# Kernel optimization log

Hardware: AMD Instinct MI355X
Metric: run time of the kernel (lower is better)

Reference implementation:

```python
import jax, jax.numpy as jnp
import numpy as np

N_NODES = 100000
N_EDGES = 1600000
FEAT = 512
CLS = 64
HID = 200  # each hop layer output width; 3 hops -> 600 concat


def spmm(row, col, vals, x):
    # out[r] = sum_{e: row[e]==r} vals[e] * x[col[e]]  -- sparse A @ x
    return jax.ops.segment_sum(x[col] * vals[:, None], row, num_segments=x.shape[0])


def setup_inputs() -> dict:
    key = jax.random.key(0)
    ks = jax.random.split(key, 12)
    adj_index = jax.random.randint(ks[0], (2, N_EDGES), 0, N_NODES, dtype=jnp.int64)
    # scale like a normalized adjacency (~1/avg_degree) to keep powers stable
    adj_values = jax.random.uniform(ks[1], (N_EDGES,), dtype=jnp.float32) * (1.0 / 16.0)
    features = jax.random.normal(ks[2], (N_NODES, FEAT), dtype=jnp.float32)
    s1 = (2.0 / (FEAT + HID)) ** 0.5
    s2 = (2.0 / (3 * HID + HID)) ** 0.5
    sf = (2.0 / (3 * HID + CLS)) ** 0.5
    W1 = jax.random.normal(ks[3], (3, FEAT, HID), dtype=jnp.float32) * s1
    b1 = jax.random.normal(ks[4], (3, HID), dtype=jnp.float32) * 0.01
    W2 = jax.random.normal(ks[5], (3, 3 * HID, HID), dtype=jnp.float32) * s2
    b2 = jax.random.normal(ks[6], (3, HID), dtype=jnp.float32) * 0.01
    Wfc = jax.random.normal(ks[7], (3 * HID, CLS), dtype=jnp.float32) * sf
    bfc = jax.random.normal(ks[8], (CLS,), dtype=jnp.float32) * 0.01
    return {"adj_index": adj_index, "adj_values": adj_values, "features": features,
            "W1": W1, "b1": b1, "W2": W2, "b2": b2, "Wfc": Wfc, "bfc": bfc}


def reference(adj_index, adj_values, features, W1, b1, W2, b2, Wfc, bfc):
    # Inference mode: dropout is identity.
    row, col = adj_index[0], adj_index[1]
    # upper (sparse) layers: linear + bias + relu, then (iterations-1) spmm hops
    outs1 = []
    for i in range(3):  # iterations = i + 1
        h = jax.nn.relu(features @ W1[i] + b1[i][None, :])
        for _ in range(i):
            h = spmm(row, col, adj_values, h)
        outs1.append(h)
    abstract1 = jnp.concatenate(outs1, axis=1)  # [N, 600]
    # bottom (dense) layers: linear, (iterations-1) spmm hops, then + bias
    outs2 = []
    for i in range(3):
        h = abstract1 @ W2[i]
        for _ in range(i):
            h = spmm(row, col, adj_values, h)
        h = h + b2[i][None, :]
        outs2.append(h)
    abstract2 = jnp.concatenate(outs2, axis=1)  # [N, 600]
    node_emb = abstract2 @ Wfc + bfc  # [N, CLS]
    predictions = jax.nn.log_softmax(node_emb, axis=1)
    return node_emb, predictions
```

## Files before the change

kernel.cpp:

```cpp
#include <hip/hip_runtime.h>

typedef unsigned short u16;
typedef unsigned int u32;
typedef __attribute__((ext_vector_type(8))) short short8;
typedef __attribute__((ext_vector_type(4))) float f32x4;
typedef __attribute__((ext_vector_type(4))) u32 u32x4;
typedef __attribute__((ext_vector_type(2))) u32 u32x2;

#define NN 100000
#define PAD 640

__device__ __forceinline__ float b2f(u16 u) {
    union { u32 i; float f; } v; v.i = ((u32)u) << 16; return v.f;
}
__device__ __forceinline__ u16 f2b(float f) {
    union { float f; u32 i; } v; v.f = f;
    u32 x = v.i;
    return (u16)((x + 0x7FFFu + ((x >> 16) & 1u)) >> 16);
}
__device__ __forceinline__ u32 pack2(float lo, float hi) {
    return (u32)f2b(lo) | ((u32)f2b(hi) << 16);
}
__device__ __forceinline__ float rdf(const void* p, size_t i, int f) {
    return f ? ((const float*)p)[i] : b2f(((const u16*)p)[i]);
}
__device__ __forceinline__ void gload16(const u16* g, u16* l) {
    __builtin_amdgcn_global_load_lds(
        (const __attribute__((address_space(1))) void*)g,
        (__attribute__((address_space(3))) void*)l, 16, 0, 0);
}

__global__ void probe_k(const int* __restrict__ idx,
                        const void* avals, const void* feats, const void* W1,
                        const void* b1, const void* W2, const void* b2,
                        const void* Wfc, const void* bfc,
                        int* __restrict__ flags) {
    if (threadIdx.x != 0 || blockIdx.x != 0) return;
    int z = 1;
    for (int i = 0; i < 128; ++i)
        if (idx[2 * i + 1] != 0) { z = 0; break; }
    flags[0] = z;
    const void* ts[8] = {avals, feats, W1, b1, W2, b2, Wfc, bfc};
    const int ns[8] = {256, 256, 256, 128, 256, 128, 256, 32};
    for (int t = 0; t < 8; ++t) {
        const u16* p = (const u16*)ts[t];
        int n = ns[t], bad = 0;
        for (int i = 0; i < n; ++i) {
            int e = (p[2 * i] >> 7) & 0xFF;
            if (e >= 133) bad++;
        }
        flags[1 + t] = (bad * 8 >= n) ? 1 : 0;
    }
}

__device__ __forceinline__ int load_row(const int* idx, int E, int f, int e) {
    return f ? idx[2 * e] : idx[e];
}
__device__ __forceinline__ int load_col(const int* idx, int E, int f, int e) {
    return f ? idx[2 * E + 2 * e] : idx[E + e];
}

__global__ void featconv_k(const void* __restrict__ src, u16* __restrict__ dst,
                           const int* __restrict__ flags) {
    int i = blockIdx.x * 256 + threadIdx.x;
    if (i >= NN * 64) return;
    int f = flags[2];
    size_t b = (size_t)i * 8;
    short8 o;
    if (f) {
        const float* sf = (const float*)src + b;
        f32x4 x0 = *(const f32x4*)sf;
        f32x4 x1 = *(const f32x4*)(sf + 4);
#pragma unroll
        for (int q = 0; q < 4; ++q) {
            o[q] = (short)f2b(x0[q]);
            o[q + 4] = (short)f2b(x1[q]);
        }
    } else {
        o = *(const short8*)((const u16*)src + b);
    }
    *(short8*)(dst + b) = o;
}
__global__ void w1t_k(const void* __restrict__ W1, u16* __restrict__ w1t,
                      const int* __restrict__ flags) {
    int i = blockIdx.x * 256 + threadIdx.x;
    if (i >= 640 * 512) return;
    int n = i >> 9, k = i & 511;
    float v = 0.f;
    if (n < 600) {
        int ib = n / 200, c = n % 200;
        v = rdf(W1, (size_t)ib * 102400 + (size_t)k * 200 + c, flags[3]);
    }
    w1t[i] = f2b(v);
}
__global__ void w2t_k(const void* __restrict__ W2, u16* __restrict__ w2t,
                      const int* __restrict__ flags) {
    int i = blockIdx.x * 256 + threadIdx.x;
    if (i >= 640 * 640) return;
    int n = i / 640, k = i % 640;
    float v = 0.f;
    if (n < 600 && k < 600) {
        int ib = n / 200, c = n % 200;
        v = rdf(W2, (size_t)ib * 120000 + (size_t)k * 200 + c, flags[5]);
    }
    w2t[i] = f2b(v);
}
__global__ void wfct_k(const void* __restrict__ Wfc, u16* __restrict__ wfct,
                       const int* __restrict__ flags) {
    int i = blockIdx.x * 256 + threadIdx.x;
    if (i >= 64 * 640) return;
    int n = i / 640, k = i % 640;
    float v = 0.f;
    if (k < 600) v = rdf(Wfc, (size_t)k * 64 + n, flags[7]);
    wfct[i] = f2b(v);
}
__global__ void bconv_k(const void* __restrict__ b1, const void* __restrict__ b2,
                        const void* __restrict__ bfc, float* __restrict__ o,
                        const int* __restrict__ flags) {
    int i = blockIdx.x * 256 + threadIdx.x;
    if (i < 600) o[i] = rdf(b1, i, flags[4]);
    else if (i < 1200) o[i] = rdf(b2, i - 600, flags[6]);
    else if (i < 1264) o[i] = rdf(bfc, i - 1200, flags[8]);
}

__device__ __forceinline__ int pad8(int c) { return (c + 7) & ~7; }

__global__ void count_k(const int* __restrict__ idx, int E, const int* __restrict__ flags,
                        int* __restrict__ counts) {
    int e = blockIdx.x * 256 + threadIdx.x;
    if (e >= E) return;
    int r = load_row(idx, E, flags[0], e);
    if ((u32)r >= NN) return;
    atomicAdd(&counts[r], 1);
}

__global__ void chunksum_k(const int* __restrict__ counts, int* __restrict__ chsum) {
    __shared__ int sm[256];
    int c = blockIdx.x, t = threadIdx.x;
    int base = c * 1024, s = 0;
    for (int i = t; i < 1024; i += 256) {
        int g = base + i;
        if (g < NN) s += pad8(counts[g]);
    }
    sm[t] = s; __syncthreads();
    for (int off = 128; off; off >>= 1) {
        if (t < off) sm[t] += sm[t + off];
        __syncthreads();
    }
    if (t == 0) chsum[c] = sm[0];
}

__global__ void chscan_k(const int* __restrict__ chsum, int nch, int* __restrict__ choff,
                         int* __restrict__ row_ptr, int E) {
    if (threadIdx.x == 0 && blockIdx.x == 0) {
        int run = 0;
        for (int c = 0; c < nch; ++c) { choff[c] = run; run += chsum[c]; }
        row_ptr[NN] = run;
    }
}

__global__ __launch_bounds__(1024) void scan_k(const int* __restrict__ counts,
                                               const int* __restrict__ choff,
                                               int* __restrict__ row_ptr,
                                               int* __restrict__ cursor) {
    __shared__ int sm[1024];
    int c = blockIdx.x, t = threadIdx.x;
    int g = c * 1024 + t;
    int v = (g < NN) ? pad8(counts[g]) : 0;
    sm[t] = v;
    __syncthreads();
    for (int off = 1; off < 1024; off <<= 1) {
        int add = (t >= off) ? sm[t - off] : 0;
        __syncthreads();
        sm[t] += add;
        __syncthreads();
    }
    if (g < NN) {
        int ex = choff[c] + sm[t] - v;
        row_ptr[g] = ex;
        cursor[g] = ex;
    }
}

__global__ void scatter_k(const int* __restrict__ idx, const void* __restrict__ avals, int E,
                          const int* __restrict__ flags, int* __restrict__ cursor,
                          int* __restrict__ edges) {
    int e = blockIdx.x * 256 + threadIdx.x;
    if (e >= E) return;
    int f = flags[0];
    int r = load_row(idx, E, f, e);
    if ((u32)r >= NN) return;
    int c = load_col(idx, E, f, e);
    if ((u32)c >= NN) c = 0;
    int p = atomicAdd(&cursor[r], 1);
    edges[2 * p] = c;
    ((float*)edges)[2 * p + 1] = rdf(avals, e, flags[1]);
}

__global__ void padfill_k(const int* __restrict__ cursor, const int* __restrict__ row_ptr,
                          int* __restrict__ edges) {
    int r = blockIdx.x * 256 + threadIdx.x;
    if (r >= NN) return;
    int p = cursor[r], e = row_ptr[r + 1];
    for (; p < e; ++p) {
        edges[2 * p] = 0;
        ((float*)edges)[2 * p + 1] = 0.f;
    }
}

__global__ __launch_bounds__(256) void gemm128_k(
    const u16* __restrict__ A, const u16* __restrict__ Bt,
    u16* __restrict__ C, float* __restrict__ Cf,
    const float* __restrict__ bias, int bias_n, int relu,
    int M, int K, int lda, int ldc) {
    __shared__ u16 As[128 * 32];
    __shared__ u16 Bs[128 * 32];
    const int tid = threadIdx.x;
    const int wave = tid >> 6, lane = tid & 63;
    const int bm = blockIdx.x * 128, bn = blockIdx.y * 128;
    const int wrow = (wave >> 1) * 64, wcol = (wave & 1) * 64;
    const int l15 = lane & 15, l4 = lane >> 4;
    f32x4 acc[4][4] = {};

    const int c0 = wave * 2;
    const int rowA0 = c0 * 16 + (lane >> 2);
    const int rowA1 = rowA0 + 16;
    const int colE = (lane & 3) * 8;
    int gr0 = bm + rowA0; if (gr0 >= M) gr0 = M - 1;
    int gr1 = bm + rowA1; if (gr1 >= M) gr1 = M - 1;
    const u16* a0p = A + (size_t)gr0 * lda + colE;
    const u16* a1p = A + (size_t)gr1 * lda + colE;
    const u16* b0p = Bt + (size_t)(bn + rowA0) * K + colE;
    const u16* b1p = Bt + (size_t)(bn + rowA1) * K + colE;
    u16* lA0 = As + c0 * 512;
    u16* lA1 = As + c0 * 512 + 512;
    u16* lB0 = Bs + c0 * 512;
    u16* lB1 = Bs + c0 * 512 + 512;

    for (int k0 = 0; k0 < K; k0 += 32) {
        __syncthreads();
        gload16(a0p + k0, lA0);
        gload16(a1p + k0, lA1);
        gload16(b0p + k0, lB0);
        gload16(b1p + k0, lB1);
        __syncthreads();
        short8 af[4], bf[4];
#pragma unroll
        for (int t = 0; t < 4; ++t) {
            af[t] = *(const short8*)&As[(wrow + t * 16 + l15) * 32 + l4 * 8];
            bf[t] = *(const short8*)&Bs[(wcol + t * 16 + l15) * 32 + l4 * 8];
        }
#pragma unroll
        for (int mi = 0; mi < 4; ++mi)
#pragma unroll
            for (int ni = 0; ni < 4; ++ni)
                acc[mi][ni] = __builtin_amdgcn_mfma_f32_16x16x32_bf16(
                    af[mi], bf[ni], acc[mi][ni], 0, 0, 0);
    }

#pragma unroll
    for (int mi = 0; mi < 4; ++mi)
#pragma unroll
        for (int ni = 0; ni < 4; ++ni)
#pragma unroll
            for (int r4 = 0; r4 < 4; ++r4) {
                int row = bm + wrow + mi * 16 + l4 * 4 + r4;
                int col = bn + wcol + ni * 16 + l15;
                if (row < M) {
                    float v = acc[mi][ni][r4];
                    if (bias && col < bias_n) v += bias[col];
                    if (relu) v = fmaxf(v, 0.0f);
                    if (C) C[(size_t)row * ldc + col] = f2b(v);
                    if (Cf) Cf[(size_t)row * ldc + col] = v;
                }
            }
}

__global__ __launch_bounds__(256) void gemm_k(
    const u16* __restrict__ A, const u16* __restrict__ Bt,
    u16* __restrict__ C, float* __restrict__ Cf,
    const float* __restrict__ bias, int bias_n, int relu,
    int M, int K, int lda, int ldc) {
    __shared__ u16 As[64][40];
    __shared__ u16 Bs[64][40];
    const int tid = threadIdx.x;
    const int wave = tid >> 6, lane = tid & 63;
    const int bm = blockIdx.x * 64, bn = blockIdx.y * 64;
    const int wr = (wave >> 1) * 32, wc = (wave & 1) * 32;
    const int l15 = lane & 15, l4 = lane >> 4;
    f32x4 acc[2][2] = {};

    const int srow = tid >> 2;
    const int skoff = (tid & 3) * 8;
    const bool arow_ok = (bm + srow) < M;
    const u16* aptr = A + (size_t)(bm + srow) * lda + skoff;
    const u16* bptr = Bt + (size_t)(bn + srow) * K + skoff;

    for (int k0 = 0; k0 < K; k0 += 32) {
        short8 av = {};
        if (arow_ok) av = *(const short8*)(aptr + k0);
        short8 bv = *(const short8*)(bptr + k0);
        __syncthreads();
        *(short8*)&As[srow][skoff] = av;
        *(short8*)&Bs[srow][skoff] = bv;
        __syncthreads();
        short8 a0 = *(const short8*)&As[wr + l15][l4 * 8];
        short8 a1 = *(const short8*)&As[wr + 16 + l15][l4 * 8];
        short8 bb0 = *(const short8*)&Bs[wc + l15][l4 * 8];
        short8 bb1 = *(const short8*)&Bs[wc + 16 + l15][l4 * 8];
        acc[0][0] = __builtin_amdgcn_mfma_f32_16x16x32_bf16(a0, bb0, acc[0][0], 0, 0, 0);
        acc[0][1] = __builtin_amdgcn_mfma_f32_16x16x32_bf16(a0, bb1, acc[0][1], 0, 0, 0);
        acc[1][0] = __builtin_amdgcn_mfma_f32_16x16x32_bf16(a1, bb0, acc[1][0], 0, 0, 0);
        acc[1][1] = __builtin_amdgcn_mfma_f32_16x16x32_bf16(a1, bb1, acc[1][1], 0, 0, 0);
    }

#pragma unroll
    for (int mi = 0; mi < 2; ++mi)
#pragma unroll
        for (int ni = 0; ni < 2; ++ni)
#pragma unroll
            for (int r = 0; r < 4; ++r) {
                int row = bm + wr + mi * 16 + l4 * 4 + r;
                int col = bn + wc + ni * 16 + l15;
                if (row < M) {
                    float v = acc[mi][ni][r];
                    if (bias && col < bias_n) v += bias[col];
                    if (relu) v = fmaxf(v, 0.0f);
                    if (C) C[(size_t)row * ldc + col] = f2b(v);
                    if (Cf) Cf[(size_t)row * ldc + col] = v;
                }
            }
}

__global__ __launch_bounds__(256) void spmm400_k(
    const int* __restrict__ row_ptr, const int* __restrict__ edges,
    const u16* __restrict__ X, u16* __restrict__ Y1, u16* __restrict__ Yt,
    const float* __restrict__ bias1) {
    int r = blockIdx.x * 4 + (threadIdx.x >> 6);
    if (r >= NN) return;
    int lane = threadIdx.x & 63;
    int s = row_ptr[r], e = row_ptr[r + 1];
    if (s < 0) s = 0;
    if (e < s) e = s;
    float a[8] = {0.f, 0.f, 0.f, 0.f, 0.f, 0.f, 0.f, 0.f};
    const bool act = lane < 50;
    const u32* xl = (const u32*)X + lane * 4;
    for (int i = s; i < e; i += 8) {
        int cc[8]; float vv[8];
#pragma unroll
        for (int j = 0; j < 4; ++j) {
            u32x4 p = *(const u32x4*)(edges + 2 * (size_t)(i + 2 * j));
            union { u32 u; float f; } w0, w1;
            cc[2 * j] = (int)p[0];     w0.u = p[1];
            cc[2 * j + 1] = (int)p[2]; w1.u = p[3];
            vv[2 * j] = w0.f; vv[2 * j + 1] = w1.f;
        }
        if (act) {
            u32x4 g[8];
#pragma unroll
            for (int j = 0; j < 8; ++j) {
                u32 c = (u32)cc[j]; if (c >= NN) c = 0;
                g[j] = *(const u32x4*)(xl + (size_t)c * 320);
            }
#pragma unroll
            for (int j = 0; j < 8; ++j) {
                float v = vv[j];
#pragma unroll
                for (int q = 0; q < 4; ++q) {
                    union { u32 i; float f; } lo, hi;
                    lo.i = g[j][q] << 16; hi.i = g[j][q] & 0xffff0000u;
                    a[2 * q] = fmaf(v, lo.f, a[2 * q]);
                    a[2 * q + 1] = fmaf(v, hi.f, a[2 * q + 1]);
                }
            }
        }
    }
    if (bias1 && lane < 25) {
#pragma unroll
        for (int q = 0; q < 8; ++q) a[q] += bias1[lane * 8 + q];
    }
    u32x4 o;
    o[0] = pack2(a[0], a[1]); o[1] = pack2(a[2], a[3]);
    o[2] = pack2(a[4], a[5]); o[3] = pack2(a[6], a[7]);
    if (lane < 25) {
        *(u32x4*)((u32*)Y1 + (size_t)r * 320 + lane * 4) = o;
    } else if (lane < 50) {
        *(u32x4*)((u32*)Yt + (size_t)r * 100 + (lane - 25) * 4) = o;
    }
}

__global__ __launch_bounds__(256) void spmm200_k(
    const int* __restrict__ row_ptr, const int* __restrict__ edges,
    const u16* __restrict__ X, int ldx,
    u16* __restrict__ Y, int ldy,
    const float* __restrict__ bias) {
    int r = blockIdx.x * 4 + (threadIdx.x >> 6);
    if (r >= NN) return;
    int lane = threadIdx.x & 63;
    int s = row_ptr[r], e = row_ptr[r + 1];
    if (s < 0) s = 0;
    if (e < s) e = s;
    float a[4] = {0.f, 0.f, 0.f, 0.f};
    const bool act = lane < 50;
    const int ldxw = ldx >> 1, ldyw = ldy >> 1;
    const u32* xl = (const u32*)X + lane * 2;
    for (int i = s; i < e; i += 8) {
        int cc[8]; float vv[8];
#pragma unroll
        for (int j = 0; j < 4; ++j) {
            u32x4 p = *(const u32x4*)(edges + 2 * (size_t)(i + 2 * j));
            union { u32 u; float f; } w0, w1;
            cc[2 * j] = (int)p[0];     w0.u = p[1];
            cc[2 * j + 1] = (int)p[2]; w1.u = p[3];
            vv[2 * j] = w0.f; vv[2 * j + 1] = w1.f;
        }
        if (act) {
            u32x2 g[8];
#pragma unroll
            for (int j = 0; j < 8; ++j) {
                u32 c = (u32)cc[j]; if (c >= NN) c = 0;
                g[j] = *(const u32x2*)(xl + (size_t)c * ldxw);
            }
#pragma unroll
            for (int j = 0; j < 8; ++j) {
                float v = vv[j];
#pragma unroll
                for (int q = 0; q < 2; ++q) {
                    union { u32 i; float f; } lo, hi;
                    lo.i = g[j][q] << 16; hi.i = g[j][q] & 0xffff0000u;
                    a[2 * q] = fmaf(v, lo.f, a[2 * q]);
                    a[2 * q + 1] = fmaf(v, hi.f, a[2 * q + 1]);
                }
            }
        }
    }
    if (bias && act) {
#pragma unroll
        for (int q = 0; q < 4; ++q) a[q] += bias[lane * 4 + q];
    }
    if (act) {
        u32x2 o;
        o[0] = pack2(a[0], a[1]); o[1] = pack2(a[2], a[3]);
        *(u32x2*)((u32*)Y + (size_t)r * ldyw + lane * 2) = o;
    }
}

__global__ void copyblk_k(const u16* __restrict__ src, u16* __restrict__ dst) {
    int i = blockIdx.x * 256 + threadIdx.x;
    if (i >= NN * 100) return;
    int r = i / 100, c = i % 100;
    ((u32*)dst)[(size_t)r * 320 + c] = ((const u32*)src)[(size_t)r * 320 + c];
}
__global__ void zeropad_k(u16* __restrict__ dst) {
    int i = blockIdx.x * 256 + threadIdx.x;
    if (i >= NN * 20) return;
    int r = i / 20, c = i % 20;
    ((u32*)dst)[(size_t)r * 320 + 300 + c] = 0u;
}
__global__ void copybias_k(const u16* __restrict__ src, u16* __restrict__ dst,
                           const float* __restrict__ bias) {
    int i = blockIdx.x * 256 + threadIdx.x;
    if (i >= NN * 200) return;
    int r = i / 200, c = i % 200;
    dst[(size_t)r * 640 + c] = f2b(b2f(src[(size_t)r * 640 + c]) + bias[c]);
}

__global__ void softmax_k(const float* __restrict__ ne, float* __restrict__ out) {
    int r = blockIdx.x * 4 + (threadIdx.x >> 6);
    if (r >= NN) return;
    int lane = threadIdx.x & 63;
    float v = ne[(size_t)r * 64 + lane];
    float m = v;
    for (int off = 32; off; off >>= 1) m = fmaxf(m, __shfl_xor(m, off, 64));
    float e = expf(v - m);
    float ssum = e;
    for (int off = 32; off; off >>= 1) ssum += __shfl_xor(ssum, off, 64);
    out[(size_t)r * 64 + lane] = v - m - logf(ssum);
}

extern "C" void kernel_launch(void* const* d_in, const int* in_sizes, int n_in,
                              void* d_out, int out_size, void* d_ws, size_t ws_size,
                              hipStream_t stream) {
    const int* adj_idx = (const int*)d_in[0];
    const void* adj_vals = d_in[1];
    const void* feats = d_in[2];
    const void* W1 = d_in[3];
    const void* b1 = d_in[4];
    const void* W2 = d_in[5];
    const void* b2 = d_in[6];
    const void* Wfc = d_in[7];
    const void* bfc = d_in[8];
    const int E = in_sizes[1];
    (void)n_in; (void)out_size; (void)ws_size;

    char* ws = (char*)d_ws;
    size_t off = 0;
    auto alloc = [&](size_t b) { size_t o = off; off += (b + 255) & ~(size_t)255; return o; };
    u16* buf0 = (u16*)(ws + alloc((size_t)NN * PAD * 2));
    u16* buf1 = (u16*)(ws + alloc((size_t)NN * PAD * 2));
    u16* hop = (u16*)(ws + alloc((size_t)NN * 200 * 2));
    u16* w1t = (u16*)(ws + alloc((size_t)640 * 512 * 2));
    u16* w2t = (u16*)(ws + alloc((size_t)640 * 640 * 2));
    u16* wfct = (u16*)(ws + alloc((size_t)64 * 640 * 2));
    float* biasf = (float*)(ws + alloc(1264 * 4));
    int* counts = (int*)(ws + alloc((size_t)NN * 4));
    int* cursor = (int*)(ws + alloc((size_t)NN * 4));
    int* row_ptr = (int*)(ws + alloc((size_t)(NN + 1) * 4));
    int* chsum = (int*)(ws + alloc(4096));
    int* choff = (int*)(ws + alloc(4096));
    int* flags = (int*)(ws + alloc(256));
    int* edgesS = (int*)(ws + alloc(((size_t)E + 8 * (size_t)NN) * 8));

    u16* featsB = buf1;
    float* out_ne = (float*)d_out;
    float* out_pred = out_ne + (size_t)NN * 64;

    probe_k<<<1, 64, 0, stream>>>(adj_idx, adj_vals, feats, W1, b1, W2, b2, Wfc, bfc, flags);
    featconv_k<<<(NN * 64 + 255) / 256, 256, 0, stream>>>(feats, featsB, flags);
    w1t_k<<<(640 * 512 + 255) / 256, 256, 0, stream>>>(W1, w1t, flags);
    w2t_k<<<(640 * 640 + 255) / 256, 256, 0, stream>>>(W2, w2t, flags);
    wfct_k<<<(64 * 640 + 255) / 256, 256, 0, stream>>>(Wfc, wfct, flags);
    bconv_k<<<5, 256, 0, stream>>>(b1, b2, bfc, biasf, flags);

    hipMemsetAsync(counts, 0, NN * 4, stream);
    count_k<<<(E + 255) / 256, 256, 0, stream>>>(adj_idx, E, flags, counts);
    const int NCH = (NN + 1023) / 1024;
    chunksum_k<<<NCH, 256, 0, stream>>>(counts, chsum);
    chscan_k<<<1, 64, 0, stream>>>(chsum, NCH, choff, row_ptr, E);
    scan_k<<<NCH, 1024, 0, stream>>>(counts, choff, row_ptr, cursor);
    scatter_k<<<(E + 255) / 256, 256, 0, stream>>>(adj_idx, adj_vals, E, flags, cursor, edgesS);
    padfill_k<<<(NN + 255) / 256, 256, 0, stream>>>(cursor, row_ptr, edgesS);

    dim3 g128((NN + 127) / 128, PAD / 128);
    gemm128_k<<<g128, 256, 0, stream>>>(featsB, w1t, buf0, nullptr, biasf, 600, 1, NN, 512, 512, PAD);
    copyblk_k<<<(NN * 100 + 255) / 256, 256, 0, stream>>>(buf0, buf1);
    zeropad_k<<<(NN * 20 + 255) / 256, 256, 0, stream>>>(buf1);
    spmm400_k<<<(NN + 3) / 4, 256, 0, stream>>>(row_ptr, edgesS,
                                                buf0 + 200, buf1 + 200, hop, nullptr);
    spmm200_k<<<(NN + 3) / 4, 256, 0, stream>>>(row_ptr, edgesS,
                                                hop, 200, buf1 + 400, PAD, nullptr);
    gemm128_k<<<g128, 256, 0, stream>>>(buf1, w2t, buf0, nullptr, nullptr, 0, 0, NN, PAD, PAD, PAD);
    copybias_k<<<(NN * 200 + 255) / 256, 256, 0, stream>>>(buf0, buf1, biasf + 600);
    spmm400_k<<<(NN + 3) / 4, 256, 0, stream>>>(row_ptr, edgesS,
                                                buf0 + 200, buf1 + 200, hop, biasf + 800);
    spmm200_k<<<(NN + 3) / 4, 256, 0, stream>>>(row_ptr, edgesS,
                                                hop, 200, buf1 + 400, PAD, biasf + 1000);
    dim3 gC((NN + 63) / 64, 1);
    gemm_k<<<gC, 256, 0, stream>>>(buf1, wfct, nullptr, out_ne, biasf + 1200, 64, 0, NN, PAD, PAD, 64);
    softmax_k<<<(NN + 3) / 4, 256, 0, stream>>>(out_ne, out_pred);
}
```

Before: 1.664 ms.

## Fuse final FC GEMM with log-softmax and merge small prep kernels

Replaces the final 64-column GEMM plus separate softmax kernel with one fc64 kernel. It uses 128-row tiles, loads tiles with global_load_lds, stages the logits in LDS and computes log-softmax in the epilogue, so the node-embedding output no longer has to be re-read from global memory. It also merges the weight-transpose and bias-conversion kernels into one 2D-grid prep kernel, merges the copy and zero-pad kernels, and parallelises the probe kernel across a wavefront. The aim is to cut launch count and an extra pass over a 100000x64 float tensor, at the cost of more LDS use and register pressure in the fused kernel.

```diff
diff --git a/kernel.cpp b/kernel.cpp
--- a/kernel.cpp
+++ b/kernel.cpp
@@ -35,21 +35,24 @@
                         const void* b1, const void* W2, const void* b2,
                         const void* Wfc, const void* bfc,
                         int* __restrict__ flags) {
-    if (threadIdx.x != 0 || blockIdx.x != 0) return;
-    int z = 1;
-    for (int i = 0; i < 128; ++i)
-        if (idx[2 * i + 1] != 0) { z = 0; break; }
-    flags[0] = z;
+    if (blockIdx.x != 0 || threadIdx.x >= 64) return;
+    int lane = threadIdx.x;
+    int v0 = idx[2 * lane + 1];
+    int v1 = idx[2 * (lane + 64) + 1];
+    int ok = (v0 == 0 && v1 == 0);
+    int allz = __all(ok);
+    if (lane == 0) flags[0] = allz ? 1 : 0;
     const void* ts[8] = {avals, feats, W1, b1, W2, b2, Wfc, bfc};
     const int ns[8] = {256, 256, 256, 128, 256, 128, 256, 32};
     for (int t = 0; t < 8; ++t) {
         const u16* p = (const u16*)ts[t];
         int n = ns[t], bad = 0;
-        for (int i = 0; i < n; ++i) {
+        for (int i = lane; i < n; i += 64) {
             int e = (p[2 * i] >> 7) & 0xFF;
             if (e >= 133) bad++;
         }
-        flags[1 + t] = (bad * 8 >= n) ? 1 : 0;
+        for (int off = 32; off; off >>= 1) bad += __shfl_xor(bad, off, 64);
+        if (lane == 0) flags[1 + t] = (bad * 8 >= n) ? 1 : 0;
     }
 }
 
@@ -81,46 +84,45 @@
     }
     *(short8*)(dst + b) = o;
 }
-__global__ void w1t_k(const void* __restrict__ W1, u16* __restrict__ w1t,
-                      const int* __restrict__ flags) {
-    int i = blockIdx.x * 256 + threadIdx.x;
-    if (i >= 640 * 512) return;
-    int n = i >> 9, k = i & 511;
-    float v = 0.f;
-    if (n < 600) {
-        int ib = n / 200, c = n % 200;
-        v = rdf(W1, (size_t)ib * 102400 + (size_t)k * 200 + c, flags[3]);
-    }
-    w1t[i] = f2b(v);
-}
-__global__ void w2t_k(const void* __restrict__ W2, u16* __restrict__ w2t,
-                      const int* __restrict__ flags) {
-    int i = blockIdx.x * 256 + threadIdx.x;
-    if (i >= 640 * 640) return;
-    int n = i / 640, k = i % 640;
-    float v = 0.f;
-    if (n < 600 && k < 600) {
-        int ib = n / 200, c = n % 200;
-        v = rdf(W2, (size_t)ib * 120000 + (size_t)k * 200 + c, flags[5]);
-    }
-    w2t[i] = f2b(v);
-}
-__global__ void wfct_k(const void* __restrict__ Wfc, u16* __restrict__ wfct,
+
+__global__ void prep_k(const void* __restrict__ W1, const void* __restrict__ W2,
+                       const void* __restrict__ Wfc,
+                       const void* __restrict__ b1, const void* __restrict__ b2,
+                       const void* __restrict__ bfc,
+                       u16* __restrict__ w1t, u16* __restrict__ w2t,
+                       u16* __restrict__ wfct, float* __restrict__ biasf,
                        const int* __restrict__ flags) {
     int i = blockIdx.x * 256 + threadIdx.x;
-    if (i >= 64 * 640) return;
-    int n = i / 640, k = i % 640;
-    float v = 0.f;
-    if (k < 600) v = rdf(Wfc, (size_t)k * 64 + n, flags[7]);
-    wfct[i] = f2b(v);
-}
-__global__ void bconv_k(const void* __restrict__ b1, const void* __restrict__ b2,
-                        const void* __restrict__ bfc, float* __restrict__ o,
-                        const int* __restrict__ flags) {
-    int i = blockIdx.x * 256 + threadIdx.x;
-    if (i < 600) o[i] = rdf(b1, i, flags[4]);
-    else if (i < 1200) o[i] = rdf(b2, i - 600, flags[6]);
-    else if (i < 1264) o[i] = rdf(bfc, i - 1200, flags[8]);
+    int job = blockIdx.y;
+    if (job == 0) {
+        if (i >= 640 * 512) return;
+        int n = i >> 9, k = i & 511;
+        float v = 0.f;
+        if (n < 600) {
+            int ib = n / 200, c = n % 200;
+            v = rdf(W1, (size_t)ib * 102400 + (size_t)k * 200 + c, flags[3]);
+        }
+        w1t[i] = f2b(v);
+    } else if (job == 1) {
+        if (i >= 640 * 640) return;
+        int n = i / 640, k = i % 640;
+        float v = 0.f;
+        if (n < 600 && k < 600) {
+            int ib = n / 200, c = n % 200;
+            v = rdf(W2, (size_t)ib * 120000 + (size_t)k * 200 + c, flags[5]);
+        }
+        w2t[i] = f2b(v);
+    } else if (job == 2) {
+        if (i >= 64 * 640) return;
+        int n = i / 640, k = i % 640;
+        float v = 0.f;
+        if (k < 600) v = rdf(Wfc, (size_t)k * 64 + n, flags[7]);
+        wfct[i] = f2b(v);
+    } else {
+        if (i < 600) biasf[i] = rdf(b1, i, flags[4]);
+        else if (i < 1200) biasf[i] = rdf(b2, i - 600, flags[6]);
+        else if (i < 1264) biasf[i] = rdf(bfc, i - 1200, flags[8]);
+    }
 }
 
 __device__ __forceinline__ int pad8(int c) { return (c + 7) & ~7; }
@@ -276,60 +278,93 @@
             }
 }
 
-__global__ __launch_bounds__(256) void gemm_k(
+__global__ __launch_bounds__(256) void fc64_k(
     const u16* __restrict__ A, const u16* __restrict__ Bt,
-    u16* __restrict__ C, float* __restrict__ Cf,
-    const float* __restrict__ bias, int bias_n, int relu,
-    int M, int K, int lda, int ldc) {
-    __shared__ u16 As[64][40];
-    __shared__ u16 Bs[64][40];
+    float* __restrict__ out_ne, float* __restrict__ out_pred,
+    const float* __restrict__ bias, int M, int K, int lda) {
+    __shared__ __align__(16) char ldsbuf[128 * 64 * 4];
+    u16* As = (u16*)ldsbuf;
+    u16* Bs = (u16*)(ldsbuf + 8192);
+    float* smC = (float*)ldsbuf;
+
     const int tid = threadIdx.x;
     const int wave = tid >> 6, lane = tid & 63;
-    const int bm = blockIdx.x * 64, bn = blockIdx.y * 64;
-    const int wr = (wave >> 1) * 32, wc = (wave & 1) * 32;
+    const int bm = blockIdx.x * 128;
+    const int wrow = (wave >> 1) * 64, wcol = (wave & 1) * 32;
     const int l15 = lane & 15, l4 = lane >> 4;
-    f32x4 acc[2][2] = {};
-
-    const int srow = tid >> 2;
-    const int skoff = (tid & 3) * 8;
-    const bool arow_ok = (bm + srow) < M;
-    const u16* aptr = A + (size_t)(bm + srow) * lda + skoff;
-    const u16* bptr = Bt + (size_t)(bn + srow) * K + skoff;
+    f32x4 acc[4][2] = {};
+
+    const int colE = (lane & 3) * 8;
+    int gr0 = bm + wave * 32 + (lane >> 2); if (gr0 >= M) gr0 = M - 1;
+    int gr1 = bm + wave * 32 + 16 + (lane >> 2); if (gr1 >= M) gr1 = M - 1;
+    const u16* a0p = A + (size_t)gr0 * lda + colE;
+    const u16* a1p = A + (size_t)gr1 * lda + colE;
+    const u16* bp = Bt + (size_t)(wave * 16 + (lane >> 2)) * K + colE;
+    u16* lA0 = As + wave * 1024;
+    u16* lA1 = As + wave * 1024 + 512;
+    u16* lB = Bs + wave * 512;
 
     for (int k0 = 0; k0 < K; k0 += 32) {
-        short8 av = {};
-        if (arow_ok) av = *(const short8*)(aptr + k0);
-        short8 bv = *(const short8*)(bptr + k0);
-        __syncthreads();
-        *(short8*)&As[srow][skoff] = av;
-        *(short8*)&Bs[srow][skoff] = bv;
-        __syncthreads();
-        short8 a0 = *(const short8*)&As[wr + l15][l4 * 8];
-        short8 a1 = *(const short8*)&As[wr + 16 + l15][l4 * 8];
-        short8 bb0 = *(const short8*)&Bs[wc + l15][l4 * 8];
-        short8 bb1 = *(const short8*)&Bs[wc + 16 + l15][l4 * 8];
-        acc[0][0] = __builtin_amdgcn_mfma_f32_16x16x32_bf16(a0, bb0, acc[0][0], 0, 0, 0);
-        acc[0][1] = __builtin_amdgcn_mfma_f32_16x16x32_bf16(a0, bb1, acc[0][1], 0, 0, 0);
-        acc[1][0] = __builtin_amdgcn_mfma_f32_16x16x32_bf16(a1, bb0, acc[1][0], 0, 0, 0);
-        acc[1][1] = __builtin_amdgcn_mfma_f32_16x16x32_bf16(a1, bb1, acc[1][1], 0, 0, 0);
-    }
-
-#pragma unroll
-    for (int mi = 0; mi < 2; ++mi)
+        __syncthreads();
+        gload16(a0p + k0, lA0);
+        gload16(a1p + k0, lA1);
+        gload16(bp + k0, lB);
+        __syncthreads();
+        short8 af[4], bf[2];
+#pragma unroll
+        for (int t = 0; t < 4; ++t)
+            af[t] = *(const short8*)&As[(wrow + t * 16 + l15) * 32 + l4 * 8];
+#pragma unroll
+        for (int t = 0; t < 2; ++t)
+            bf[t] = *(const short8*)&Bs[(wcol + t * 16 + l15) * 32 + l4 * 8];
+#pragma unroll
+        for (int mi = 0; mi < 4; ++mi)
+#pragma unroll
+            for (int ni = 0; ni < 2; ++ni)
+                acc[mi][ni] = __builtin_amdgcn_mfma_f32_16x16x32_bf16(
+                    af[mi], bf[ni], acc[mi][ni], 0, 0, 0);
+    }
+
+    __syncthreads();
+#pragma unroll
+    for (int mi = 0; mi < 4; ++mi)
 #pragma unroll
         for (int ni = 0; ni < 2; ++ni)
 #pragma unroll
-            for (int r = 0; r < 4; ++r) {
-                int row = bm + wr + mi * 16 + l4 * 4 + r;
-                int col = bn + wc + ni * 16 + l15;
-                if (row < M) {
-                    float v = acc[mi][ni][r];
-                    if (bias && col < bias_n) v += bias[col];
-                    if (relu) v = fmaxf(v, 0.0f);
-                    if (C) C[(size_t)row * ldc + col] = f2b(v);
-                    if (Cf) Cf[(size_t)row * ldc + col] = v;
-                }
+            for (int r4 = 0; r4 < 4; ++r4) {
+                int rl = wrow + mi * 16 + l4 * 4 + r4;
+                int col = wcol + ni * 16 + l15;
+                int row = bm + rl;
+                float v = acc[mi][ni][r4] + bias[col];
+                smC[rl * 64 + col] = v;
+                if (row < M) out_ne[(size_t)row * 64 + col] = v;
             }
+    __syncthreads();
+
+    const int rl = tid >> 1, half = tid & 1;
+    const int row = bm + rl;
+    float vv[32];
+#pragma unroll
+    for (int k = 0; k < 32; ++k) {
+        int c = half * 32 + ((k + rl) & 31);
+        vv[k] = smC[rl * 64 + c];
+    }
+    float m = vv[0];
+#pragma unroll
+    for (int k = 1; k < 32; ++k) m = fmaxf(m, vv[k]);
+    m = fmaxf(m, __shfl_xor(m, 1, 64));
+    float s = 0.f;
+#pragma unroll
+    for (int k = 0; k < 32; ++k) s += expf(vv[k] - m);
+    s += __shfl_xor(s, 1, 64);
+    float lg = m + logf(s);
+    if (row < M) {
+#pragma unroll
+        for (int k = 0; k < 32; ++k) {
+            int c = half * 32 + ((k + rl) & 31);
+            out_pred[(size_t)row * 64 + c] = vv[k] - lg;
+        }
+    }
 }
 
 __global__ __launch_bounds__(256) void spmm400_k(
@@ -445,17 +480,14 @@
     }
 }
 
-__global__ void copyblk_k(const u16* __restrict__ src, u16* __restrict__ dst) {
+__global__ void copypad_k(const u16* __restrict__ src, u16* __restrict__ dst) {
     int i = blockIdx.x * 256 + threadIdx.x;
-    if (i >= NN * 100) return;
-    int r = i / 100, c = i % 100;
-    ((u32*)dst)[(size_t)r * 320 + c] = ((const u32*)src)[(size_t)r * 320 + c];
-}
-__global__ void zeropad_k(u16* __restrict__ dst) {
-    int i = blockIdx.x * 256 + threadIdx.x;
-    if (i >= NN * 20) return;
-    int r = i / 20, c = i % 20;
-    ((u32*)dst)[(size_t)r * 320 + 300 + c] = 0u;
+    if (i >= NN * 120) return;
+    int r = i / 120, c = i % 120;
+    if (c < 100)
+        ((u32*)dst)[(size_t)r * 320 + c] = ((const u32*)src)[(size_t)r * 320 + c];
+    else
+        ((u32*)dst)[(size_t)r * 320 + 300 + (c - 100)] = 0u;
 }
 __global__ void copybias_k(const u16* __restrict__ src, u16* __restrict__ dst,
                            const float* __restrict__ bias) {
@@ -463,19 +495,6 @@
     if (i >= NN * 200) return;
     int r = i / 200, c = i % 200;
     dst[(size_t)r * 640 + c] = f2b(b2f(src[(size_t)r * 640 + c]) + bias[c]);
-}
-
-__global__ void softmax_k(const float* __restrict__ ne, float* __restrict__ out) {
-    int r = blockIdx.x * 4 + (threadIdx.x >> 6);
-    if (r >= NN) return;
-    int lane = threadIdx.x & 63;
-    float v = ne[(size_t)r * 64 + lane];
-    float m = v;
-    for (int off = 32; off; off >>= 1) m = fmaxf(m, __shfl_xor(m, off, 64));
-    float e = expf(v - m);
-    float ssum = e;
-    for (int off = 32; off; off >>= 1) ssum += __shfl_xor(ssum, off, 64);
-    out[(size_t)r * 64 + lane] = v - m - logf(ssum);
 }
 
 extern "C" void kernel_launch(void* const* d_in, const int* in_sizes, int n_in,
@@ -517,10 +536,8 @@
 
     probe_k<<<1, 64, 0, stream>>>(adj_idx, adj_vals, feats, W1, b1, W2, b2, Wfc, bfc, flags);
     featconv_k<<<(NN * 64 + 255) / 256, 256, 0, stream>>>(feats, featsB, flags);
-    w1t_k<<<(640 * 512 + 255) / 256, 256, 0, stream>>>(W1, w1t, flags);
-    w2t_k<<<(640 * 640 + 255) / 256, 256, 0, stream>>>(W2, w2t, flags);
-    wfct_k<<<(64 * 640 + 255) / 256, 256, 0, stream>>>(Wfc, wfct, flags);
-    bconv_k<<<5, 256, 0, stream>>>(b1, b2, bfc, biasf, flags);
+    dim3 gp(1600, 4);
+    prep_k<<<gp, 256, 0, stream>>>(W1, W2, Wfc, b1, b2, bfc, w1t, w2t, wfct, biasf, flags);
 
     hipMemsetAsync(counts, 0, NN * 4, stream);
     count_k<<<(E + 255) / 256, 256, 0, stream>>>(adj_idx, E, flags, counts);
@@ -533,8 +550,7 @@
 
     dim3 g128((NN + 127) / 128, PAD / 128);
     gemm128_k<<<g128, 256, 0, stream>>>(featsB, w1t, buf0, nullptr, biasf, 600, 1, NN, 512, 512, PAD);
-    copyblk_k<<<(NN * 100 + 255) / 256, 256, 0, stream>>>(buf0, buf1);
-    zeropad_k<<<(NN * 20 + 255) / 256, 256, 0, stream>>>(buf1);
+    copypad_k<<<(NN * 120 + 255) / 256, 256, 0, stream>>>(buf0, buf1);
     spmm400_k<<<(NN + 3) / 4, 256, 0, stream>>>(row_ptr, edgesS,
                                                 buf0 + 200, buf1 + 200, hop, nullptr);
     spmm200_k<<<(NN + 3) / 4, 256, 0, stream>>>(row_ptr, edgesS,
@@ -545,7 +561,6 @@
                                                 buf0 + 200, buf1 + 200, hop, biasf + 800);
     spmm200_k<<<(NN + 3) / 4, 256, 0, stream>>>(row_ptr, edgesS,
                                                 hop, 200, buf1 + 400, PAD, biasf + 1000);
-    dim3 gC((NN + 63) / 64, 1);
-    gemm_k<<<gC, 256, 0, stream>>>(buf1, wfct, nullptr, out_ne, biasf + 1200, 64, 0, NN, PAD, PAD, 64);
-    softmax_k<<<(NN + 3) / 4, 256, 0, stream>>>(out_ne, out_pred);
-}
+    fc64_k<<<(NN + 127) / 128, 256, 0, stream>>>(buf1, wfct, out_ne, out_pred,
+                                                 biasf + 1200, NN, PAD, PAD);
+}
```

New measurement: 1.589 ms. -4.5%, faster.
